# Performance work log

Measured on AMD Instinct MI355X. Metric: run time of the kernel, lower is better.

The kernel has to match this reference:

```python
import jax, jax.numpy as jnp
import numpy as np
import math

TEXT_EMBEDDING_DIM = 768.0
SEQ = 81
DIM = 64
B, H = 256, 16


def setup_inputs() -> dict:
    key = jax.random.key(0)
    kq, kk, kv, ke = jax.random.split(key, 4)
    Q = jax.random.normal(kq, (B, H, SEQ, DIM), dtype=jnp.float32)
    K = jax.random.normal(kk, (B, H, SEQ, DIM), dtype=jnp.float32)
    V = jax.random.normal(kv, (B, H, SEQ, DIM), dtype=jnp.float32)
    emb_table = jax.random.normal(ke, (2 * SEQ + 1, DIM), dtype=jnp.float32)
    return {"Q": Q, "K": K, "V": V, "emb_table": emb_table, "use_causal": 1}


def reference(Q, K, V, emb_table, use_causal):
    S = Q.shape[-2]
    # relative index matrix: rel[i, j] = (S - 1 + i) - j, in [0, 2S-2]
    rel = jnp.arange(S - 1, 2 * S - 1)[:, None] - jnp.arange(S)  # [S, S] int
    emb = emb_table[rel]  # [S, S, d]
    # QK^T plus learned relative-position bias
    eij = jnp.einsum('bhid,bhjd->bhij', Q, K) + jnp.einsum('bhid,ijd->bhij', Q, emb)
    attn = eij / math.sqrt(TEXT_EMBEDDING_DIM)  # note: sqrt(768), not sqrt(dim), per source
    if use_causal:
        i = jnp.arange(S)[:, None]
        j = jnp.arange(S)
        mask = jnp.where(i >= j, 0.0, -1000000000.0).astype(attn.dtype)  # [S, S]
        attn = attn + mask
    attn = jax.nn.softmax(attn, axis=-1)
    return jnp.einsum('bhij,bhjd->bhid', attn, V)
```

## Files before the change

### kernel.cpp

```cpp
#include <hip/hip_runtime.h>
#include <hip/hip_bf16.h>

#define SEQ 81
#define DIM 64
#define NT  384
#define NW  6
#define LDK 68
#define LDV 100
#define LDP 100

typedef short bf16x8 __attribute__((ext_vector_type(8)));
typedef short bf16x4 __attribute__((ext_vector_type(4)));
typedef float f32x4  __attribute__((ext_vector_type(4)));

static constexpr float kS2 = 0.0520587716f;

__device__ __forceinline__ short f2bf(float f) {
    __hip_bfloat16 h = __float2bfloat16(f);
    return __builtin_bit_cast(short, h);
}
__device__ __forceinline__ float bf2f(short h) {
    unsigned u = ((unsigned)(unsigned short)h) << 16;
    return __builtin_bit_cast(float, u);
}
__device__ __forceinline__ bf16x8 cat8(bf16x4 a, bf16x4 b) {
    bf16x8 r;
    r[0]=a[0]; r[1]=a[1]; r[2]=a[2]; r[3]=a[3];
    r[4]=b[0]; r[5]=b[1]; r[6]=b[2]; r[7]=b[3];
    return r;
}

__global__ void emb_cvt_kernel(const float* __restrict__ in, short* __restrict__ out, int n) {
    int i = blockIdx.x * 256 + threadIdx.x;
    if (i < n) out[i] = f2bf(in[i]);
}

__global__ __launch_bounds__(NT, 8)
void rpsa_kernel(const float* __restrict__ Q, const float* __restrict__ K,
                 const float* __restrict__ V, const short* __restrict__ embw,
                 const int* __restrict__ ucp, float* __restrict__ out)
{
    extern __shared__ char smraw[];
    short* sVt = (short*)smraw;
    short* sK  = (short*)(smraw + 12800);
    short* sP  = (short*)(smraw + 12800);

    const int tid = threadIdx.x;
    const size_t base = (size_t)blockIdx.x * (SEQ * DIM);
    const int uc = ucp[0];
    const int w  = tid >> 6, L = tid & 63;
    const int lr = L & 15,  lg = L >> 4;
    const int iRow = 16*w + lr;

    bf16x8 aq0, aq1;
    {
        const int qrow = (iRow < SEQ) ? iRow : (SEQ - 1);
        const float* qp = Q + base + qrow*DIM + 8*lg;
        const f32x4 q0 = *(const f32x4*)(qp);
        const f32x4 q1 = *(const f32x4*)(qp + 4);
        const f32x4 q2 = *(const f32x4*)(qp + 32);
        const f32x4 q3 = *(const f32x4*)(qp + 36);
        #pragma unroll
        for (int t = 0; t < 4; ++t) {
            aq0[t]   = f2bf(q0[t]*kS2);
            aq0[4+t] = f2bf(q1[t]*kS2);
            aq1[t]   = f2bf(q2[t]*kS2);
            aq1[4+t] = f2bf(q3[t]*kS2);
        }
    }

    for (int u = tid; u < 96 * DIM / 8; u += NT) {
        const int row = u >> 3, so = (u & 7) * 8;
        bf16x4 lo = {0,0,0,0}, hi = {0,0,0,0};
        if (row < SEQ) {
            const f32x4 k0 = *(const f32x4*)(K + base + row*DIM + so);
            const f32x4 k1 = *(const f32x4*)(K + base + row*DIM + so + 4);
            #pragma unroll
            for (int t = 0; t < 4; ++t) { lo[t] = f2bf(k0[t]); hi[t] = f2bf(k1[t]); }
        }
        *(bf16x4*)(sK + row*LDK + so)     = lo;
        *(bf16x4*)(sK + row*LDK + so + 4) = hi;
    }
    {
        const int j4 = tid >> 4;
        const int d4 = tid & 15;
        f32x4 rw[4];
        #pragma unroll
        for (int e = 0; e < 4; ++e) {
            const int j = 4*j4 + e;
            rw[e] = (j < SEQ) ? *(const f32x4*)(V + base + j*DIM + 4*d4)
                              : (f32x4){0.f,0.f,0.f,0.f};
        }
        #pragma unroll
        for (int c = 0; c < 4; ++c) {
            const int d = 4*d4 + c;
            bf16x4 pv = { f2bf(rw[0][c]), f2bf(rw[1][c]), f2bf(rw[2][c]), f2bf(rw[3][c]) };
            *(bf16x4*)(sVt + d*LDV + 4*j4) = pv;
        }
    }

    bf16x4 qe[NW];
    #pragma unroll
    for (int nt2 = 0; nt2 < NW; ++nt2) {
        if (nt2 > w) continue;
        int erow = 80 + 16*nt2 + lr;
        if (erow > 2*SEQ) erow = 2*SEQ;
        bf16x8 e0 = *(const bf16x8*)(embw + erow*DIM + 8*lg);
        bf16x8 e1 = *(const bf16x8*)(embw + erow*DIM + 32 + 8*lg);
        f32x4 a = {0.f,0.f,0.f,0.f};
        a = __builtin_amdgcn_mfma_f32_16x16x32_bf16(e0, aq0, a, 0, 0, 0);
        a = __builtin_amdgcn_mfma_f32_16x16x32_bf16(e1, aq1, a, 0, 0, 0);
        bf16x4 p = { f2bf(a[0]), f2bf(a[1]), f2bf(a[2]), f2bf(a[3]) };
        qe[nt2] = p;
    }
    __syncthreads();

    f32x4 accs[NW] = {};
    const int ntEnd = uc ? w : (NW - 1);
    #pragma unroll
    for (int nt = 0; nt < NW; ++nt) {
        if (nt > ntEnd) continue;
        const int kr = 16*nt + lr;
        bf16x8 b0 = cat8(*(const bf16x4*)(sK + kr*LDK + 8*lg),
                         *(const bf16x4*)(sK + kr*LDK + 8*lg + 4));
        bf16x8 b1 = cat8(*(const bf16x4*)(sK + kr*LDK + 32 + 8*lg),
                         *(const bf16x4*)(sK + kr*LDK + 32 + 8*lg + 4));
        f32x4 a = accs[nt];
        a = __builtin_amdgcn_mfma_f32_16x16x32_bf16(b0, aq0, a, 0, 0, 0);
        a = __builtin_amdgcn_mfma_f32_16x16x32_bf16(b1, aq1, a, 0, 0, 0);
        accs[nt] = a;
    }
    __syncthreads();

    #pragma unroll
    for (int nt2 = 0; nt2 < NW; ++nt2) {
        if (nt2 > w) continue;
        #pragma unroll
        for (int r = 0; r < 4; ++r) {
            const int j = 16*(w - nt2) + lr - 4*lg - r;
            if (j >= 0) sP[iRow*LDP + j] = qe[nt2][r];
        }
    }
    if (!uc) {
        #pragma unroll
        for (int nt2 = 0; nt2 < NW - 1; ++nt2) {
            if (nt2 < w) continue;
            const int erow = 16*nt2 + lr;
            bf16x8 e0 = *(const bf16x8*)(embw + erow*DIM + 8*lg);
            bf16x8 e1 = *(const bf16x8*)(embw + erow*DIM + 32 + 8*lg);
            f32x4 a = {0.f,0.f,0.f,0.f};
            a = __builtin_amdgcn_mfma_f32_16x16x32_bf16(e0, aq0, a, 0, 0, 0);
            a = __builtin_amdgcn_mfma_f32_16x16x32_bf16(e1, aq1, a, 0, 0, 0);
            #pragma unroll
            for (int r = 0; r < 4; ++r) {
                const int rel = 16*nt2 + 4*lg + r;
                if (rel >= iRow) sP[iRow*LDP + (80 + iRow - rel)] = f2bf(a[r]);
            }
        }
    }

    const int jmax = uc ? ((iRow < SEQ-1) ? iRow : SEQ-1) : (SEQ-1);
    float sum = 0.f;
    #pragma unroll
    for (int nt = 0; nt < NW; ++nt) {
        short* slot = sP + iRow*LDP + 16*nt + 4*lg;
        if (nt <= ntEnd) {
            bf16x4 bias = *(const bf16x4*)(slot);
            bf16x4 p;
            #pragma unroll
            for (int r = 0; r < 4; ++r) {
                const int j = 16*nt + 4*lg + r;
                const float x = accs[nt][r] + bf2f(bias[r]);
                const float e = (j <= jmax) ? exp2f(x) : 0.f;
                sum += e;
                p[r] = f2bf(e);
            }
            *(bf16x4*)(slot) = p;
        } else {
            *(bf16x4*)(slot) = (bf16x4){0,0,0,0};
        }
    }
    sum += __shfl_xor(sum, 16);
    sum += __shfl_xor(sum, 32);
    const float inv = 1.f / sum;

    const int nks = uc ? ((w >> 1) + 1) : 3;
    bf16x8 ap0, ap1, ap2;
    ap0 = cat8(*(const bf16x4*)(sP + iRow*LDP + 8*lg),
               *(const bf16x4*)(sP + iRow*LDP + 8*lg + 4));
    if (nks > 1)
        ap1 = cat8(*(const bf16x4*)(sP + iRow*LDP + 32 + 8*lg),
                   *(const bf16x4*)(sP + iRow*LDP + 32 + 8*lg + 4));
    if (nks > 2)
        ap2 = cat8(*(const bf16x4*)(sP + iRow*LDP + 64 + 8*lg),
                   *(const bf16x4*)(sP + iRow*LDP + 64 + 8*lg + 4));
    #pragma unroll
    for (int nt = 0; nt < 4; ++nt) {
        const int d = 16*nt + lr;
        f32x4 a = {0.f,0.f,0.f,0.f};
        bf16x8 b0 = cat8(*(const bf16x4*)(sVt + d*LDV + 8*lg),
                         *(const bf16x4*)(sVt + d*LDV + 8*lg + 4));
        a = __builtin_amdgcn_mfma_f32_16x16x32_bf16(b0, ap0, a, 0, 0, 0);
        if (nks > 1) {
            bf16x8 b1 = cat8(*(const bf16x4*)(sVt + d*LDV + 32 + 8*lg),
                             *(const bf16x4*)(sVt + d*LDV + 32 + 8*lg + 4));
            a = __builtin_amdgcn_mfma_f32_16x16x32_bf16(b1, ap1, a, 0, 0, 0);
        }
        if (nks > 2) {
            bf16x8 b2 = cat8(*(const bf16x4*)(sVt + d*LDV + 64 + 8*lg),
                             *(const bf16x4*)(sVt + d*LDV + 64 + 8*lg + 4));
            a = __builtin_amdgcn_mfma_f32_16x16x32_bf16(b2, ap2, a, 0, 0, 0);
        }
        if (iRow < SEQ) {
            f32x4 o = { a[0]*inv, a[1]*inv, a[2]*inv, a[3]*inv };
            *(f32x4*)(out + base + iRow*DIM + 16*nt + 4*lg) = o;
        }
    }
}

extern "C" void kernel_launch(void* const* d_in, const int* in_sizes, int n_in,
                              void* d_out, int out_size, void* d_ws, size_t ws_size,
                              hipStream_t stream) {
    const float* Q   = (const float*)d_in[0];
    const float* K   = (const float*)d_in[1];
    const float* V   = (const float*)d_in[2];
    const float* emb = (const float*)d_in[3];
    const int*   uc  = (const int*)d_in[4];
    float* out = (float*)d_out;

    const int nbh   = in_sizes[0] / (SEQ * DIM);
    const int n_emb = in_sizes[3];

    short* embw = (short*)d_ws;
    emb_cvt_kernel<<<(n_emb + 255) / 256, 256, 0, stream>>>(emb, embw, n_emb);

    const size_t smem = 32000;
    hipFuncSetAttribute(reinterpret_cast<const void*>(rpsa_kernel),
                        hipFuncAttributeMaxDynamicSharedMemorySize, (int)smem);
    rpsa_kernel<<<nbh, NT, smem, stream>>>(Q, K, V, embw, uc, out);
}
```

Baseline: 83.99 us.

## Process four heads per block with register prefetch of next head's Q/K/V

```diff
diff --git a/kernel.cpp b/kernel.cpp
--- a/kernel.cpp
+++ b/kernel.cpp
@@ -5,6 +5,7 @@
 #define DIM 64
 #define NT  384
 #define NW  6
+#define HPB 4
 #define LDK 68
 #define LDV 100
 #define LDP 100
@@ -35,10 +36,10 @@
     if (i < n) out[i] = f2bf(in[i]);
 }
 
-__global__ __launch_bounds__(NT, 8)
+__global__ __launch_bounds__(NT, 4)
 void rpsa_kernel(const float* __restrict__ Q, const float* __restrict__ K,
                  const float* __restrict__ V, const short* __restrict__ embw,
-                 const int* __restrict__ ucp, float* __restrict__ out)
+                 const int* __restrict__ ucp, float* __restrict__ out, int nbh)
 {
     extern __shared__ char smraw[];
     short* sVt = (short*)smraw;
@@ -46,176 +47,191 @@
     short* sP  = (short*)(smraw + 12800);
 
     const int tid = threadIdx.x;
-    const size_t base = (size_t)blockIdx.x * (SEQ * DIM);
     const int uc = ucp[0];
     const int w  = tid >> 6, L = tid & 63;
     const int lr = L & 15,  lg = L >> 4;
     const int iRow = 16*w + lr;
-
-    bf16x8 aq0, aq1;
-    {
-        const int qrow = (iRow < SEQ) ? iRow : (SEQ - 1);
-        const float* qp = Q + base + qrow*DIM + 8*lg;
-        const f32x4 q0 = *(const f32x4*)(qp);
-        const f32x4 q1 = *(const f32x4*)(qp + 4);
-        const f32x4 q2 = *(const f32x4*)(qp + 32);
-        const f32x4 q3 = *(const f32x4*)(qp + 36);
-        #pragma unroll
-        for (int t = 0; t < 4; ++t) {
-            aq0[t]   = f2bf(q0[t]*kS2);
-            aq0[4+t] = f2bf(q1[t]*kS2);
-            aq1[t]   = f2bf(q2[t]*kS2);
-            aq1[4+t] = f2bf(q3[t]*kS2);
-        }
+    const int qrow = (iRow < SEQ) ? iRow : (SEQ - 1);
+    const int krow0 = tid >> 3;
+    const int krow1 = krow0 + 48;
+    const int kso   = (tid & 7) * 8;
+    const int j4 = tid >> 4, d4 = tid & 15;
+
+    const f32x4 zero4 = {0.f, 0.f, 0.f, 0.f};
+    f32x4 pq0, pq1, pq2, pq3;
+    f32x4 pk0, pk1, pk2, pk3;
+    f32x4 pv0, pv1, pv2, pv3;
+
+#define LOAD_HEAD(B)                                                              \
+    {                                                                             \
+        const float* qp = Q + (B) + qrow*DIM + 8*lg;                              \
+        pq0 = *(const f32x4*)(qp);      pq1 = *(const f32x4*)(qp + 4);            \
+        pq2 = *(const f32x4*)(qp + 32); pq3 = *(const f32x4*)(qp + 36);           \
+        pk0 = *(const f32x4*)(K + (B) + krow0*DIM + kso);                         \
+        pk1 = *(const f32x4*)(K + (B) + krow0*DIM + kso + 4);                     \
+        pk2 = (krow1 < SEQ) ? *(const f32x4*)(K + (B) + krow1*DIM + kso)     : zero4; \
+        pk3 = (krow1 < SEQ) ? *(const f32x4*)(K + (B) + krow1*DIM + kso + 4) : zero4; \
+        pv0 = (4*j4+0 < SEQ) ? *(const f32x4*)(V + (B) + (4*j4+0)*DIM + 4*d4) : zero4; \
+        pv1 = (4*j4+1 < SEQ) ? *(const f32x4*)(V + (B) + (4*j4+1)*DIM + 4*d4) : zero4; \
+        pv2 = (4*j4+2 < SEQ) ? *(const f32x4*)(V + (B) + (4*j4+2)*DIM + 4*d4) : zero4; \
+        pv3 = (4*j4+3 < SEQ) ? *(const f32x4*)(V + (B) + (4*j4+3)*DIM + 4*d4) : zero4; \
     }
 
-    for (int u = tid; u < 96 * DIM / 8; u += NT) {
-        const int row = u >> 3, so = (u & 7) * 8;
-        bf16x4 lo = {0,0,0,0}, hi = {0,0,0,0};
-        if (row < SEQ) {
-            const f32x4 k0 = *(const f32x4*)(K + base + row*DIM + so);
-            const f32x4 k1 = *(const f32x4*)(K + base + row*DIM + so + 4);
-            #pragma unroll
-            for (int t = 0; t < 4; ++t) { lo[t] = f2bf(k0[t]); hi[t] = f2bf(k1[t]); }
-        }
-        *(bf16x4*)(sK + row*LDK + so)     = lo;
-        *(bf16x4*)(sK + row*LDK + so + 4) = hi;
-    }
-    {
-        const int j4 = tid >> 4;
-        const int d4 = tid & 15;
-        f32x4 rw[4];
-        #pragma unroll
-        for (int e = 0; e < 4; ++e) {
-            const int j = 4*j4 + e;
-            rw[e] = (j < SEQ) ? *(const f32x4*)(V + base + j*DIM + 4*d4)
-                              : (f32x4){0.f,0.f,0.f,0.f};
+    int h = blockIdx.x * HPB;
+    LOAD_HEAD((size_t)h * (SEQ * DIM));
+
+    for (int hh = 0; hh < HPB; ++hh, ++h) {
+        if (h >= nbh) break;
+        const size_t base = (size_t)h * (SEQ * DIM);
+
+        {
+            bf16x4 lo, hi;
+            #pragma unroll
+            for (int t = 0; t < 4; ++t) { lo[t] = f2bf(pk0[t]); hi[t] = f2bf(pk1[t]); }
+            *(bf16x4*)(sK + krow0*LDK + kso)     = lo;
+            *(bf16x4*)(sK + krow0*LDK + kso + 4) = hi;
+            #pragma unroll
+            for (int t = 0; t < 4; ++t) { lo[t] = f2bf(pk2[t]); hi[t] = f2bf(pk3[t]); }
+            *(bf16x4*)(sK + krow1*LDK + kso)     = lo;
+            *(bf16x4*)(sK + krow1*LDK + kso + 4) = hi;
         }
         #pragma unroll
         for (int c = 0; c < 4; ++c) {
             const int d = 4*d4 + c;
-            bf16x4 pv = { f2bf(rw[0][c]), f2bf(rw[1][c]), f2bf(rw[2][c]), f2bf(rw[3][c]) };
-            *(bf16x4*)(sVt + d*LDV + 4*j4) = pv;
-        }
-    }
-
-    bf16x4 qe[NW];
-    #pragma unroll
-    for (int nt2 = 0; nt2 < NW; ++nt2) {
-        if (nt2 > w) continue;
-        int erow = 80 + 16*nt2 + lr;
-        if (erow > 2*SEQ) erow = 2*SEQ;
-        bf16x8 e0 = *(const bf16x8*)(embw + erow*DIM + 8*lg);
-        bf16x8 e1 = *(const bf16x8*)(embw + erow*DIM + 32 + 8*lg);
-        f32x4 a = {0.f,0.f,0.f,0.f};
-        a = __builtin_amdgcn_mfma_f32_16x16x32_bf16(e0, aq0, a, 0, 0, 0);
-        a = __builtin_amdgcn_mfma_f32_16x16x32_bf16(e1, aq1, a, 0, 0, 0);
-        bf16x4 p = { f2bf(a[0]), f2bf(a[1]), f2bf(a[2]), f2bf(a[3]) };
-        qe[nt2] = p;
-    }
-    __syncthreads();
-
-    f32x4 accs[NW] = {};
-    const int ntEnd = uc ? w : (NW - 1);
-    #pragma unroll
-    for (int nt = 0; nt < NW; ++nt) {
-        if (nt > ntEnd) continue;
-        const int kr = 16*nt + lr;
-        bf16x8 b0 = cat8(*(const bf16x4*)(sK + kr*LDK + 8*lg),
-                         *(const bf16x4*)(sK + kr*LDK + 8*lg + 4));
-        bf16x8 b1 = cat8(*(const bf16x4*)(sK + kr*LDK + 32 + 8*lg),
-                         *(const bf16x4*)(sK + kr*LDK + 32 + 8*lg + 4));
-        f32x4 a = accs[nt];
-        a = __builtin_amdgcn_mfma_f32_16x16x32_bf16(b0, aq0, a, 0, 0, 0);
-        a = __builtin_amdgcn_mfma_f32_16x16x32_bf16(b1, aq1, a, 0, 0, 0);
-        accs[nt] = a;
-    }
-    __syncthreads();
-
-    #pragma unroll
-    for (int nt2 = 0; nt2 < NW; ++nt2) {
-        if (nt2 > w) continue;
-        #pragma unroll
-        for (int r = 0; r < 4; ++r) {
-            const int j = 16*(w - nt2) + lr - 4*lg - r;
-            if (j >= 0) sP[iRow*LDP + j] = qe[nt2][r];
-        }
-    }
-    if (!uc) {
-        #pragma unroll
-        for (int nt2 = 0; nt2 < NW - 1; ++nt2) {
-            if (nt2 < w) continue;
-            const int erow = 16*nt2 + lr;
+            bf16x4 pvv = { f2bf(pv0[c]), f2bf(pv1[c]), f2bf(pv2[c]), f2bf(pv3[c]) };
+            *(bf16x4*)(sVt + d*LDV + 4*j4) = pvv;
+        }
+        bf16x8 aq0, aq1;
+        #pragma unroll
+        for (int t = 0; t < 4; ++t) {
+            aq0[t]   = f2bf(pq0[t]*kS2);
+            aq0[4+t] = f2bf(pq1[t]*kS2);
+            aq1[t]   = f2bf(pq2[t]*kS2);
+            aq1[4+t] = f2bf(pq3[t]*kS2);
+        }
+        if (hh + 1 < HPB && h + 1 < nbh)
+            LOAD_HEAD((size_t)(h + 1) * (SEQ * DIM));
+
+        bf16x4 qe[NW];
+        #pragma unroll
+        for (int nt2 = 0; nt2 < NW; ++nt2) {
+            if (nt2 > w) continue;
+            int erow = 80 + 16*nt2 + lr;
+            if (erow > 2*SEQ) erow = 2*SEQ;
             bf16x8 e0 = *(const bf16x8*)(embw + erow*DIM + 8*lg);
             bf16x8 e1 = *(const bf16x8*)(embw + erow*DIM + 32 + 8*lg);
             f32x4 a = {0.f,0.f,0.f,0.f};
             a = __builtin_amdgcn_mfma_f32_16x16x32_bf16(e0, aq0, a, 0, 0, 0);
             a = __builtin_amdgcn_mfma_f32_16x16x32_bf16(e1, aq1, a, 0, 0, 0);
+            bf16x4 p = { f2bf(a[0]), f2bf(a[1]), f2bf(a[2]), f2bf(a[3]) };
+            qe[nt2] = p;
+        }
+        __syncthreads();
+
+        f32x4 accs[NW] = {};
+        const int ntEnd = uc ? w : (NW - 1);
+        #pragma unroll
+        for (int nt = 0; nt < NW; ++nt) {
+            if (nt > ntEnd) continue;
+            const int kr = 16*nt + lr;
+            bf16x8 b0 = cat8(*(const bf16x4*)(sK + kr*LDK + 8*lg),
+                             *(const bf16x4*)(sK + kr*LDK + 8*lg + 4));
+            bf16x8 b1 = cat8(*(const bf16x4*)(sK + kr*LDK + 32 + 8*lg),
+                             *(const bf16x4*)(sK + kr*LDK + 32 + 8*lg + 4));
+            f32x4 a = accs[nt];
+            a = __builtin_amdgcn_mfma_f32_16x16x32_bf16(b0, aq0, a, 0, 0, 0);
+            a = __builtin_amdgcn_mfma_f32_16x16x32_bf16(b1, aq1, a, 0, 0, 0);
+            accs[nt] = a;
+        }
+        __syncthreads();
+
+        #pragma unroll
+        for (int nt2 = 0; nt2 < NW; ++nt2) {
+            if (nt2 > w) continue;
             #pragma unroll
             for (int r = 0; r < 4; ++r) {
-                const int rel = 16*nt2 + 4*lg + r;
-                if (rel >= iRow) sP[iRow*LDP + (80 + iRow - rel)] = f2bf(a[r]);
-            }
-        }
+                const int j = 16*(w - nt2) + lr - 4*lg - r;
+                if (j >= 0) sP[iRow*LDP + j] = qe[nt2][r];
+            }
+        }
+        if (!uc) {
+            #pragma unroll
+            for (int nt2 = 0; nt2 < NW - 1; ++nt2) {
+                if (nt2 < w) continue;
+                const int erow = 16*nt2 + lr;
+                bf16x8 e0 = *(const bf16x8*)(embw + erow*DIM + 8*lg);
+                bf16x8 e1 = *(const bf16x8*)(embw + erow*DIM + 32 + 8*lg);
+                f32x4 a = {0.f,0.f,0.f,0.f};
+                a = __builtin_amdgcn_mfma_f32_16x16x32_bf16(e0, aq0, a, 0, 0, 0);
+                a = __builtin_amdgcn_mfma_f32_16x16x32_bf16(e1, aq1, a, 0, 0, 0);
+                #pragma unroll
+                for (int r = 0; r < 4; ++r) {
+                    const int rel = 16*nt2 + 4*lg + r;
+                    if (rel >= iRow) sP[iRow*LDP + (80 + iRow - rel)] = f2bf(a[r]);
+                }
+            }
+        }
+
+        const int jmax = uc ? ((iRow < SEQ-1) ? iRow : SEQ-1) : (SEQ-1);
+        float sum = 0.f;
+        #pragma unroll
+        for (int nt = 0; nt < NW; ++nt) {
+            short* slot = sP + iRow*LDP + 16*nt + 4*lg;
+            if (nt <= ntEnd) {
+                bf16x4 bias = *(const bf16x4*)(slot);
+                bf16x4 p;
+                #pragma unroll
+                for (int r = 0; r < 4; ++r) {
+                    const int j = 16*nt + 4*lg + r;
+                    const float x = accs[nt][r] + bf2f(bias[r]);
+                    const float e = (j <= jmax) ? exp2f(x) : 0.f;
+                    sum += e;
+                    p[r] = f2bf(e);
+                }
+                *(bf16x4*)(slot) = p;
+            } else {
+                *(bf16x4*)(slot) = (bf16x4){0,0,0,0};
+            }
+        }
+        sum += __shfl_xor(sum, 16);
+        sum += __shfl_xor(sum, 32);
+        const float inv = 1.f / sum;
+
+        const int nks = uc ? ((w >> 1) + 1) : 3;
+        bf16x8 ap0, ap1, ap2;
+        ap0 = cat8(*(const bf16x4*)(sP + iRow*LDP + 8*lg),
+                   *(const bf16x4*)(sP + iRow*LDP + 8*lg + 4));
+        if (nks > 1)
+            ap1 = cat8(*(const bf16x4*)(sP + iRow*LDP + 32 + 8*lg),
+                       *(const bf16x4*)(sP + iRow*LDP + 32 + 8*lg + 4));
+        if (nks > 2)
+            ap2 = cat8(*(const bf16x4*)(sP + iRow*LDP + 64 + 8*lg),
+                       *(const bf16x4*)(sP + iRow*LDP + 64 + 8*lg + 4));
+        #pragma unroll
+        for (int nt = 0; nt < 4; ++nt) {
+            const int d = 16*nt + lr;
+            f32x4 a = {0.f,0.f,0.f,0.f};
+            bf16x8 b0 = cat8(*(const bf16x4*)(sVt + d*LDV + 8*lg),
+                             *(const bf16x4*)(sVt + d*LDV + 8*lg + 4));
+            a = __builtin_amdgcn_mfma_f32_16x16x32_bf16(b0, ap0, a, 0, 0, 0);
+            if (nks > 1) {
+                bf16x8 b1 = cat8(*(const bf16x4*)(sVt + d*LDV + 32 + 8*lg),
+                                 *(const bf16x4*)(sVt + d*LDV + 32 + 8*lg + 4));
+                a = __builtin_amdgcn_mfma_f32_16x16x32_bf16(b1, ap1, a, 0, 0, 0);
+            }
+            if (nks > 2) {
+                bf16x8 b2 = cat8(*(const bf16x4*)(sVt + d*LDV + 64 + 8*lg),
+                                 *(const bf16x4*)(sVt + d*LDV + 64 + 8*lg + 4));
+                a = __builtin_amdgcn_mfma_f32_16x16x32_bf16(b2, ap2, a, 0, 0, 0);
+            }
+            if (iRow < SEQ) {
+                f32x4 o = { a[0]*inv, a[1]*inv, a[2]*inv, a[3]*inv };
+                *(f32x4*)(out + base + iRow*DIM + 16*nt + 4*lg) = o;
+            }
+        }
+        __syncthreads();
     }
-
-    const int jmax = uc ? ((iRow < SEQ-1) ? iRow : SEQ-1) : (SEQ-1);
-    float sum = 0.f;
-    #pragma unroll
-    for (int nt = 0; nt < NW; ++nt) {
-        short* slot = sP + iRow*LDP + 16*nt + 4*lg;
-        if (nt <= ntEnd) {
-            bf16x4 bias = *(const bf16x4*)(slot);
-            bf16x4 p;
-            #pragma unroll
-            for (int r = 0; r < 4; ++r) {
-                const int j = 16*nt + 4*lg + r;
-                const float x = accs[nt][r] + bf2f(bias[r]);
-                const float e = (j <= jmax) ? exp2f(x) : 0.f;
-                sum += e;
-                p[r] = f2bf(e);
-            }
-            *(bf16x4*)(slot) = p;
-        } else {
-            *(bf16x4*)(slot) = (bf16x4){0,0,0,0};
-        }
-    }
-    sum += __shfl_xor(sum, 16);
-    sum += __shfl_xor(sum, 32);
-    const float inv = 1.f / sum;
-
-    const int nks = uc ? ((w >> 1) + 1) : 3;
-    bf16x8 ap0, ap1, ap2;
-    ap0 = cat8(*(const bf16x4*)(sP + iRow*LDP + 8*lg),
-               *(const bf16x4*)(sP + iRow*LDP + 8*lg + 4));
-    if (nks > 1)
-        ap1 = cat8(*(const bf16x4*)(sP + iRow*LDP + 32 + 8*lg),
-                   *(const bf16x4*)(sP + iRow*LDP + 32 + 8*lg + 4));
-    if (nks > 2)
-        ap2 = cat8(*(const bf16x4*)(sP + iRow*LDP + 64 + 8*lg),
-                   *(const bf16x4*)(sP + iRow*LDP + 64 + 8*lg + 4));
-    #pragma unroll
-    for (int nt = 0; nt < 4; ++nt) {
-        const int d = 16*nt + lr;
-        f32x4 a = {0.f,0.f,0.f,0.f};
-        bf16x8 b0 = cat8(*(const bf16x4*)(sVt + d*LDV + 8*lg),
-                         *(const bf16x4*)(sVt + d*LDV + 8*lg + 4));
-        a = __builtin_amdgcn_mfma_f32_16x16x32_bf16(b0, ap0, a, 0, 0, 0);
-        if (nks > 1) {
-            bf16x8 b1 = cat8(*(const bf16x4*)(sVt + d*LDV + 32 + 8*lg),
-                             *(const bf16x4*)(sVt + d*LDV + 32 + 8*lg + 4));
-            a = __builtin_amdgcn_mfma_f32_16x16x32_bf16(b1, ap1, a, 0, 0, 0);
-        }
-        if (nks > 2) {
-            bf16x8 b2 = cat8(*(const bf16x4*)(sVt + d*LDV + 64 + 8*lg),
-                             *(const bf16x4*)(sVt + d*LDV + 64 + 8*lg + 4));
-            a = __builtin_amdgcn_mfma_f32_16x16x32_bf16(b2, ap2, a, 0, 0, 0);
-        }
-        if (iRow < SEQ) {
-            f32x4 o = { a[0]*inv, a[1]*inv, a[2]*inv, a[3]*inv };
-            *(f32x4*)(out + base + iRow*DIM + 16*nt + 4*lg) = o;
-        }
-    }
+#undef LOAD_HEAD
 }
 
 extern "C" void kernel_launch(void* const* d_in, const int* in_sizes, int n_in,
@@ -234,8 +250,9 @@
     short* embw = (short*)d_ws;
     emb_cvt_kernel<<<(n_emb + 255) / 256, 256, 0, stream>>>(emb, embw, n_emb);
 
+    const int grid = (nbh + HPB - 1) / HPB;
     const size_t smem = 32000;
     hipFuncSetAttribute(reinterpret_cast<const void*>(rpsa_kernel),
                         hipFuncAttributeMaxDynamicSharedMemorySize, (int)smem);
-    rpsa_kernel<<<nbh, NT, smem, stream>>>(Q, K, V, embw, uc, out);
-}
+    rpsa_kernel<<<grid, NT, smem, stream>>>(Q, K, V, embw, uc, out, nbh);
+}
```

New measurement: 174.1 us. 2.07x slower.

## Halve block size and pair complementary row tiles per wave for causal balance

Applied to the files above, without the earlier changes.

```diff
diff --git a/kernel.cpp b/kernel.cpp
--- a/kernel.cpp
+++ b/kernel.cpp
@@ -3,7 +3,7 @@
 
 #define SEQ 81
 #define DIM 64
-#define NT  384
+#define NT  192
 #define NW  6
 #define LDK 68
 #define LDV 100
@@ -32,10 +32,10 @@
 
 __global__ void emb_cvt_kernel(const float* __restrict__ in, short* __restrict__ out, int n) {
     int i = blockIdx.x * 256 + threadIdx.x;
-    if (i < n) out[i] = f2bf(in[i]);
-}
-
-__global__ __launch_bounds__(NT, 8)
+    if (i < n) out[i] = f2bf(i < n ? in[i] : 0.f);
+}
+
+__global__ __launch_bounds__(NT, 4)
 void rpsa_kernel(const float* __restrict__ Q, const float* __restrict__ K,
                  const float* __restrict__ V, const short* __restrict__ embw,
                  const int* __restrict__ ucp, float* __restrict__ out)
@@ -50,11 +50,15 @@
     const int uc = ucp[0];
     const int w  = tid >> 6, L = tid & 63;
     const int lr = L & 15,  lg = L >> 4;
-    const int iRow = 16*w + lr;
-
-    bf16x8 aq0, aq1;
-    {
-        const int qrow = (iRow < SEQ) ? iRow : (SEQ - 1);
+    const int bnd[2] = { w, 5 - w };
+    int iR[2];
+    iR[0] = 16*bnd[0] + lr;
+    iR[1] = 16*bnd[1] + lr;
+
+    bf16x8 aq[2][2];
+    #pragma unroll
+    for (int b = 0; b < 2; ++b) {
+        const int qrow = (iR[b] < SEQ) ? iR[b] : (SEQ - 1);
         const float* qp = Q + base + qrow*DIM + 8*lg;
         const f32x4 q0 = *(const f32x4*)(qp);
         const f32x4 q1 = *(const f32x4*)(qp + 4);
@@ -62,10 +66,10 @@
         const f32x4 q3 = *(const f32x4*)(qp + 36);
         #pragma unroll
         for (int t = 0; t < 4; ++t) {
-            aq0[t]   = f2bf(q0[t]*kS2);
-            aq0[4+t] = f2bf(q1[t]*kS2);
-            aq1[t]   = f2bf(q2[t]*kS2);
-            aq1[4+t] = f2bf(q3[t]*kS2);
+            aq[b][0][t]   = f2bf(q0[t]*kS2);
+            aq[b][0][4+t] = f2bf(q1[t]*kS2);
+            aq[b][1][t]   = f2bf(q2[t]*kS2);
+            aq[b][1][4+t] = f2bf(q3[t]*kS2);
         }
     }
 
@@ -81,9 +85,9 @@
         *(bf16x4*)(sK + row*LDK + so)     = lo;
         *(bf16x4*)(sK + row*LDK + so + 4) = hi;
     }
-    {
-        const int j4 = tid >> 4;
-        const int d4 = tid & 15;
+    for (int u = tid; u < 384; u += NT) {
+        const int j4 = u >> 4;
+        const int d4 = u & 15;
         f32x4 rw[4];
         #pragma unroll
         for (int e = 0; e < 4; ++e) {
@@ -99,121 +103,142 @@
         }
     }
 
-    bf16x4 qe[NW];
-    #pragma unroll
-    for (int nt2 = 0; nt2 < NW; ++nt2) {
-        if (nt2 > w) continue;
-        int erow = 80 + 16*nt2 + lr;
-        if (erow > 2*SEQ) erow = 2*SEQ;
-        bf16x8 e0 = *(const bf16x8*)(embw + erow*DIM + 8*lg);
-        bf16x8 e1 = *(const bf16x8*)(embw + erow*DIM + 32 + 8*lg);
-        f32x4 a = {0.f,0.f,0.f,0.f};
-        a = __builtin_amdgcn_mfma_f32_16x16x32_bf16(e0, aq0, a, 0, 0, 0);
-        a = __builtin_amdgcn_mfma_f32_16x16x32_bf16(e1, aq1, a, 0, 0, 0);
-        bf16x4 p = { f2bf(a[0]), f2bf(a[1]), f2bf(a[2]), f2bf(a[3]) };
-        qe[nt2] = p;
-    }
-    __syncthreads();
-
-    f32x4 accs[NW] = {};
-    const int ntEnd = uc ? w : (NW - 1);
-    #pragma unroll
-    for (int nt = 0; nt < NW; ++nt) {
-        if (nt > ntEnd) continue;
-        const int kr = 16*nt + lr;
-        bf16x8 b0 = cat8(*(const bf16x4*)(sK + kr*LDK + 8*lg),
-                         *(const bf16x4*)(sK + kr*LDK + 8*lg + 4));
-        bf16x8 b1 = cat8(*(const bf16x4*)(sK + kr*LDK + 32 + 8*lg),
-                         *(const bf16x4*)(sK + kr*LDK + 32 + 8*lg + 4));
-        f32x4 a = accs[nt];
-        a = __builtin_amdgcn_mfma_f32_16x16x32_bf16(b0, aq0, a, 0, 0, 0);
-        a = __builtin_amdgcn_mfma_f32_16x16x32_bf16(b1, aq1, a, 0, 0, 0);
-        accs[nt] = a;
-    }
-    __syncthreads();
-
-    #pragma unroll
-    for (int nt2 = 0; nt2 < NW; ++nt2) {
-        if (nt2 > w) continue;
-        #pragma unroll
-        for (int r = 0; r < 4; ++r) {
-            const int j = 16*(w - nt2) + lr - 4*lg - r;
-            if (j >= 0) sP[iRow*LDP + j] = qe[nt2][r];
-        }
-    }
-    if (!uc) {
-        #pragma unroll
-        for (int nt2 = 0; nt2 < NW - 1; ++nt2) {
-            if (nt2 < w) continue;
-            const int erow = 16*nt2 + lr;
+    bf16x4 qe[2][NW];
+    #pragma unroll
+    for (int b = 0; b < 2; ++b) {
+        #pragma unroll
+        for (int nt2 = 0; nt2 < NW; ++nt2) {
+            if (nt2 > bnd[b]) continue;
+            int erow = 80 + 16*nt2 + lr;
+            if (erow > 2*SEQ) erow = 2*SEQ;
             bf16x8 e0 = *(const bf16x8*)(embw + erow*DIM + 8*lg);
             bf16x8 e1 = *(const bf16x8*)(embw + erow*DIM + 32 + 8*lg);
             f32x4 a = {0.f,0.f,0.f,0.f};
-            a = __builtin_amdgcn_mfma_f32_16x16x32_bf16(e0, aq0, a, 0, 0, 0);
-            a = __builtin_amdgcn_mfma_f32_16x16x32_bf16(e1, aq1, a, 0, 0, 0);
+            a = __builtin_amdgcn_mfma_f32_16x16x32_bf16(e0, aq[b][0], a, 0, 0, 0);
+            a = __builtin_amdgcn_mfma_f32_16x16x32_bf16(e1, aq[b][1], a, 0, 0, 0);
+            bf16x4 p = { f2bf(a[0]), f2bf(a[1]), f2bf(a[2]), f2bf(a[3]) };
+            qe[b][nt2] = p;
+        }
+    }
+    __syncthreads();
+
+    f32x4 accs[2][NW] = {};
+    int ntEnd[2];
+    ntEnd[0] = uc ? bnd[0] : (NW - 1);
+    ntEnd[1] = uc ? bnd[1] : (NW - 1);
+    #pragma unroll
+    for (int b = 0; b < 2; ++b) {
+        #pragma unroll
+        for (int nt = 0; nt < NW; ++nt) {
+            if (nt > ntEnd[b]) continue;
+            const int kr = 16*nt + lr;
+            bf16x8 b0 = cat8(*(const bf16x4*)(sK + kr*LDK + 8*lg),
+                             *(const bf16x4*)(sK + kr*LDK + 8*lg + 4));
+            bf16x8 b1 = cat8(*(const bf16x4*)(sK + kr*LDK + 32 + 8*lg),
+                             *(const bf16x4*)(sK + kr*LDK + 32 + 8*lg + 4));
+            f32x4 a = accs[b][nt];
+            a = __builtin_amdgcn_mfma_f32_16x16x32_bf16(b0, aq[b][0], a, 0, 0, 0);
+            a = __builtin_amdgcn_mfma_f32_16x16x32_bf16(b1, aq[b][1], a, 0, 0, 0);
+            accs[b][nt] = a;
+        }
+    }
+    __syncthreads();
+
+    #pragma unroll
+    for (int b = 0; b < 2; ++b) {
+        #pragma unroll
+        for (int nt2 = 0; nt2 < NW; ++nt2) {
+            if (nt2 > bnd[b]) continue;
             #pragma unroll
             for (int r = 0; r < 4; ++r) {
-                const int rel = 16*nt2 + 4*lg + r;
-                if (rel >= iRow) sP[iRow*LDP + (80 + iRow - rel)] = f2bf(a[r]);
-            }
-        }
-    }
-
-    const int jmax = uc ? ((iRow < SEQ-1) ? iRow : SEQ-1) : (SEQ-1);
-    float sum = 0.f;
-    #pragma unroll
-    for (int nt = 0; nt < NW; ++nt) {
-        short* slot = sP + iRow*LDP + 16*nt + 4*lg;
-        if (nt <= ntEnd) {
-            bf16x4 bias = *(const bf16x4*)(slot);
-            bf16x4 p;
+                const int j = iR[b] - 16*nt2 - 4*lg - r;
+                if (j >= 0) sP[iR[b]*LDP + j] = qe[b][nt2][r];
+            }
+        }
+    }
+    if (!uc) {
+        #pragma unroll
+        for (int b = 0; b < 2; ++b) {
             #pragma unroll
-            for (int r = 0; r < 4; ++r) {
-                const int j = 16*nt + 4*lg + r;
-                const float x = accs[nt][r] + bf2f(bias[r]);
-                const float e = (j <= jmax) ? exp2f(x) : 0.f;
-                sum += e;
-                p[r] = f2bf(e);
-            }
-            *(bf16x4*)(slot) = p;
-        } else {
-            *(bf16x4*)(slot) = (bf16x4){0,0,0,0};
-        }
-    }
-    sum += __shfl_xor(sum, 16);
-    sum += __shfl_xor(sum, 32);
-    const float inv = 1.f / sum;
-
-    const int nks = uc ? ((w >> 1) + 1) : 3;
-    bf16x8 ap0, ap1, ap2;
-    ap0 = cat8(*(const bf16x4*)(sP + iRow*LDP + 8*lg),
-               *(const bf16x4*)(sP + iRow*LDP + 8*lg + 4));
-    if (nks > 1)
-        ap1 = cat8(*(const bf16x4*)(sP + iRow*LDP + 32 + 8*lg),
-                   *(const bf16x4*)(sP + iRow*LDP + 32 + 8*lg + 4));
-    if (nks > 2)
-        ap2 = cat8(*(const bf16x4*)(sP + iRow*LDP + 64 + 8*lg),
-                   *(const bf16x4*)(sP + iRow*LDP + 64 + 8*lg + 4));
-    #pragma unroll
-    for (int nt = 0; nt < 4; ++nt) {
-        const int d = 16*nt + lr;
-        f32x4 a = {0.f,0.f,0.f,0.f};
-        bf16x8 b0 = cat8(*(const bf16x4*)(sVt + d*LDV + 8*lg),
-                         *(const bf16x4*)(sVt + d*LDV + 8*lg + 4));
-        a = __builtin_amdgcn_mfma_f32_16x16x32_bf16(b0, ap0, a, 0, 0, 0);
-        if (nks > 1) {
-            bf16x8 b1 = cat8(*(const bf16x4*)(sVt + d*LDV + 32 + 8*lg),
-                             *(const bf16x4*)(sVt + d*LDV + 32 + 8*lg + 4));
-            a = __builtin_amdgcn_mfma_f32_16x16x32_bf16(b1, ap1, a, 0, 0, 0);
-        }
-        if (nks > 2) {
-            bf16x8 b2 = cat8(*(const bf16x4*)(sVt + d*LDV + 64 + 8*lg),
-                             *(const bf16x4*)(sVt + d*LDV + 64 + 8*lg + 4));
-            a = __builtin_amdgcn_mfma_f32_16x16x32_bf16(b2, ap2, a, 0, 0, 0);
-        }
-        if (iRow < SEQ) {
-            f32x4 o = { a[0]*inv, a[1]*inv, a[2]*inv, a[3]*inv };
-            *(f32x4*)(out + base + iRow*DIM + 16*nt + 4*lg) = o;
+            for (int nt2 = 0; nt2 < NW - 1; ++nt2) {
+                if (nt2 < bnd[b]) continue;
+                const int erow = 16*nt2 + lr;
+                bf16x8 e0 = *(const bf16x8*)(embw + erow*DIM + 8*lg);
+                bf16x8 e1 = *(const bf16x8*)(embw + erow*DIM + 32 + 8*lg);
+                f32x4 a = {0.f,0.f,0.f,0.f};
+                a = __builtin_amdgcn_mfma_f32_16x16x32_bf16(e0, aq[b][0], a, 0, 0, 0);
+                a = __builtin_amdgcn_mfma_f32_16x16x32_bf16(e1, aq[b][1], a, 0, 0, 0);
+                #pragma unroll
+                for (int r = 0; r < 4; ++r) {
+                    const int rel = 16*nt2 + 4*lg + r;
+                    if (rel >= iR[b]) sP[iR[b]*LDP + (80 + iR[b] - rel)] = f2bf(a[r]);
+                }
+            }
+        }
+    }
+
+    float inv[2];
+    #pragma unroll
+    for (int b = 0; b < 2; ++b) {
+        const int jmax = uc ? ((iR[b] < SEQ-1) ? iR[b] : SEQ-1) : (SEQ-1);
+        float sum = 0.f;
+        #pragma unroll
+        for (int nt = 0; nt < NW; ++nt) {
+            short* slot = sP + iR[b]*LDP + 16*nt + 4*lg;
+            if (nt <= ntEnd[b]) {
+                bf16x4 bias = *(const bf16x4*)(slot);
+                bf16x4 p;
+                #pragma unroll
+                for (int r = 0; r < 4; ++r) {
+                    const int j = 16*nt + 4*lg + r;
+                    const float x = accs[b][nt][r] + bf2f(bias[r]);
+                    const float e = (j <= jmax) ? exp2f(x) : 0.f;
+                    sum += e;
+                    p[r] = f2bf(e);
+                }
+                *(bf16x4*)(slot) = p;
+            } else {
+                *(bf16x4*)(slot) = (bf16x4){0,0,0,0};
+            }
+        }
+        sum += __shfl_xor(sum, 16);
+        sum += __shfl_xor(sum, 32);
+        inv[b] = 1.f / sum;
+    }
+
+    #pragma unroll
+    for (int b = 0; b < 2; ++b) {
+        const int nks = uc ? ((bnd[b] >> 1) + 1) : 3;
+        bf16x8 ap0, ap1, ap2;
+        ap0 = cat8(*(const bf16x4*)(sP + iR[b]*LDP + 8*lg),
+                   *(const bf16x4*)(sP + iR[b]*LDP + 8*lg + 4));
+        if (nks > 1)
+            ap1 = cat8(*(const bf16x4*)(sP + iR[b]*LDP + 32 + 8*lg),
+                       *(const bf16x4*)(sP + iR[b]*LDP + 32 + 8*lg + 4));
+        if (nks > 2)
+            ap2 = cat8(*(const bf16x4*)(sP + iR[b]*LDP + 64 + 8*lg),
+                       *(const bf16x4*)(sP + iR[b]*LDP + 64 + 8*lg + 4));
+        #pragma unroll
+        for (int nt = 0; nt < 4; ++nt) {
+            const int d = 16*nt + lr;
+            f32x4 a = {0.f,0.f,0.f,0.f};
+            bf16x8 b0 = cat8(*(const bf16x4*)(sVt + d*LDV + 8*lg),
+                             *(const bf16x4*)(sVt + d*LDV + 8*lg + 4));
+            a = __builtin_amdgcn_mfma_f32_16x16x32_bf16(b0, ap0, a, 0, 0, 0);
+            if (nks > 1) {
+                bf16x8 b1 = cat8(*(const bf16x4*)(sVt + d*LDV + 32 + 8*lg),
+                                 *(const bf16x4*)(sVt + d*LDV + 32 + 8*lg + 4));
+                a = __builtin_amdgcn_mfma_f32_16x16x32_bf16(b1, ap1, a, 0, 0, 0);
+            }
+            if (nks > 2) {
+                bf16x8 b2 = cat8(*(const bf16x4*)(sVt + d*LDV + 64 + 8*lg),
+                                 *(const bf16x4*)(sVt + d*LDV + 64 + 8*lg + 4));
+                a = __builtin_amdgcn_mfma_f32_16x16x32_bf16(b2, ap2, a, 0, 0, 0);
+            }
+            if (iR[b] < SEQ) {
+                f32x4 o = { a[0]*inv[b], a[1]*inv[b], a[2]*inv[b], a[3]*inv[b] };
+                *(f32x4*)(out + base + iR[b]*DIM + 16*nt + 4*lg) = o;
+            }
         }
     }
 }
```

After: 98.23 us. 1.17x slower.
